# Performance work log

Measured on AMD Instinct MI355X. Metric: run time of the kernel, lower is better.

Reference implementation:

```python
import jax, jax.numpy as jnp
import numpy as np

N_SPEC = 256
M_IN = 16384
K_OUT = 4096


def _get_edges(wl):
    # bin edges at midpoints, extrapolated half a bin at each end
    mid = (wl[1:] + wl[:-1]) / 2
    first = wl[0] - (wl[1] - wl[0]) / 2
    last = wl[-1] + (wl[-1] - wl[-2]) / 2
    return jnp.concatenate([first[None], mid, last[None]])


def setup_inputs() -> dict:
    key = jax.random.key(0)
    k1, = jax.random.split(key, 1)
    # strictly increasing wavelength grids (nm); output grid coarser and inside input range
    wl_in = jnp.linspace(400.0, 900.0, M_IN, dtype=jnp.float32)
    wl_out = jnp.linspace(405.0, 895.0, K_OUT, dtype=jnp.float32)
    flux_in = jax.random.uniform(k1, (N_SPEC, M_IN), dtype=jnp.float32, minval=0.1, maxval=1.0)
    return {"wl_in": wl_in, "flux_in": flux_in, "wl_out": wl_out}


def reference(wl_in, flux_in, wl_out):
    # Flux-conserving rebinning (Spectrum.resample with method='conserve').
    edges_in = _get_edges(wl_in)    # (M+1,)
    edges_out = _get_edges(wl_out)  # (K+1,)
    delta_in = edges_in[1:] - edges_in[:-1]    # (M,)
    delta_out = edges_out[1:] - edges_out[:-1]  # (K,)
    # overlap length between each output bin k and input bin m -> (K, M)
    overlap_lo = jnp.maximum(edges_out[:-1, None], edges_in[None, :-1])
    overlap_hi = jnp.minimum(edges_out[1:, None], edges_in[None, 1:])
    overlap = jnp.clip(overlap_hi - overlap_lo, 0, None)
    frac = overlap / delta_in[None, :]  # fraction of input bin m landing in output bin k
    # sum_m flux[n,m] * frac[k,m] * delta_in[m]  (contraction instead of the (N,K,M) broadcast)
    w = frac * delta_in[None, :]  # (K, M)
    flux_out = jnp.einsum('nm,km->nk', flux_in, w) / delta_out[None, :]
    return flux_out
```

## Files before the change

kernel.cpp:

```cpp
#include <hip/hip_runtime.h>


#define MAXW 6
#define NPB  8

__device__ __forceinline__ float edge_at(const float* __restrict__ wl, int n, int m) {
    if (m <= 0) return wl[0] - 0.5f * (wl[1] - wl[0]);
    if (m >= n) return wl[n - 1] + 0.5f * (wl[n - 1] - wl[n - 2]);
    return 0.5f * (wl[m - 1] + wl[m]);
}

__global__ __launch_bounds__(256) void rebin_kernel(
    const float* __restrict__ wl_in, const float* __restrict__ flux_in,
    const float* __restrict__ wl_out, float* __restrict__ out,
    int M, int K, int N)
{
    int k = blockIdx.x * blockDim.x + threadIdx.x;
    if (k >= K) return;

    float eo_lo = edge_at(wl_out, K, k);
    float eo_hi = edge_at(wl_out, K, k + 1);
    float inv_d = 1.0f / (eo_hi - eo_lo);

    int lo = 0, hi = M;
    while (lo < hi) {
        int mid = (lo + hi) >> 1;
        if (edge_at(wl_in, M, mid + 1) <= eo_lo) lo = mid + 1; else hi = mid;
    }
    int m0 = lo;

    float w[MAXW];
    int   mi[MAXW];
    #pragma unroll
    for (int j = 0; j < MAXW; ++j) {
        int m = m0 + j;
        float ww = 0.0f;
        if (m < M) {
            float a = edge_at(wl_in, M, m);
            float b = edge_at(wl_in, M, m + 1);
            ww = fmaxf(fminf(eo_hi, b) - fmaxf(eo_lo, a), 0.0f) * inv_d;
        }
        w[j]  = ww;
        mi[j] = (m < M) ? m : (M - 1);
    }

    int n0   = blockIdx.y * NPB;
    int nend = min(n0 + NPB, N);
    for (int n = n0; n < nend; ++n) {
        const float* fr = flux_in + (size_t)n * M;
        float acc = 0.0f;
        #pragma unroll
        for (int j = 0; j < MAXW; ++j) acc = fmaf(fr[mi[j]], w[j], acc);
        out[(size_t)n * K + k] = acc;
    }
}

extern "C" void kernel_launch(void* const* d_in, const int* in_sizes, int n_in,
                              void* d_out, int out_size, void* d_ws, size_t ws_size,
                              hipStream_t stream) {
    const float* wl_in   = (const float*)d_in[0];
    const float* flux_in = (const float*)d_in[1];
    const float* wl_out  = (const float*)d_in[2];
    float* out = (float*)d_out;

    int M = in_sizes[0];
    int K = in_sizes[2];
    int N = in_sizes[1] / M;

    dim3 block(256);
    dim3 grid((K + 255) / 256, (N + NPB - 1) / NPB);
    rebin_kernel<<<grid, block, 0, stream>>>(wl_in, flux_in, wl_out, out, M, K, N);
}
```

Measured before the change: 77.02 us.

## Replace binary search with arithmetic bin estimate and vectorized aligned loads

Computes the starting input bin from an assumed uniform spacing, then corrects it with short linear walks instead of a dependent-load binary search. Weights are built over an 8-wide window aligned to 4 so flux can be read with two float4 loads. Rows per block drop from 8 to 2 to raise parallelism, at the cost of repeating per-thread setup more often. The walks stay correct for non-uniform grids but could get long there.

Measured after the change: 73.34 us. -4.8%, faster.

```diff
diff --git a/kernel.cpp b/kernel.cpp
--- a/kernel.cpp
+++ b/kernel.cpp
@@ -1,8 +1,7 @@
 #include <hip/hip_runtime.h>
 
 
-#define MAXW 6
-#define NPB  8
+#define NPB 2
 
 __device__ __forceinline__ float edge_at(const float* __restrict__ wl, int n, int m) {
     if (m <= 0) return wl[0] - 0.5f * (wl[1] - wl[0]);
@@ -10,7 +9,7 @@
     return 0.5f * (wl[m - 1] + wl[m]);
 }
 
-__global__ __launch_bounds__(256) void rebin_kernel(
+__global__ __launch_bounds__(256) void rebin_v2_kernel(
     const float* __restrict__ wl_in, const float* __restrict__ flux_in,
     const float* __restrict__ wl_out, float* __restrict__ out,
     int M, int K, int N)
@@ -22,35 +21,51 @@
     float eo_hi = edge_at(wl_out, K, k + 1);
     float inv_d = 1.0f / (eo_hi - eo_lo);
 
-    int lo = 0, hi = M;
-    while (lo < hi) {
-        int mid = (lo + hi) >> 1;
-        if (edge_at(wl_in, M, mid + 1) <= eo_lo) lo = mid + 1; else hi = mid;
-    }
-    int m0 = lo;
+    float w0 = wl_in[0];
+    float e0 = w0 - 0.5f * (wl_in[1] - w0);
+    float spacing = (wl_in[M - 1] - w0) / (float)(M - 1);
+    int m0 = (int)floorf((eo_lo - e0) / spacing);
+    m0 = max(0, min(M - 1, m0));
+    while (m0 > 0 && edge_at(wl_in, M, m0) > eo_lo) --m0;
+    while (m0 < M - 1 && edge_at(wl_in, M, m0 + 1) <= eo_lo) ++m0;
 
-    float w[MAXW];
-    int   mi[MAXW];
+    int abase = m0 & ~3;
+
+    float wa[8];
+    float e_prev = edge_at(wl_in, M, abase);
     #pragma unroll
-    for (int j = 0; j < MAXW; ++j) {
-        int m = m0 + j;
-        float ww = 0.0f;
-        if (m < M) {
-            float a = edge_at(wl_in, M, m);
-            float b = edge_at(wl_in, M, m + 1);
-            ww = fmaxf(fminf(eo_hi, b) - fmaxf(eo_lo, a), 0.0f) * inv_d;
-        }
-        w[j]  = ww;
-        mi[j] = (m < M) ? m : (M - 1);
+    for (int t = 0; t < 8; ++t) {
+        float e_next = edge_at(wl_in, M, abase + t + 1);
+        float ov = fminf(eo_hi, e_next) - fmaxf(eo_lo, e_prev);
+        wa[t] = fmaxf(ov, 0.0f) * inv_d;
+        e_prev = e_next;
     }
 
     int n0   = blockIdx.y * NPB;
     int nend = min(n0 + NPB, N);
+    bool fast = (abase + 8 <= M);
     for (int n = n0; n < nend; ++n) {
         const float* fr = flux_in + (size_t)n * M;
-        float acc = 0.0f;
-        #pragma unroll
-        for (int j = 0; j < MAXW; ++j) acc = fmaf(fr[mi[j]], w[j], acc);
+        float acc;
+        if (fast) {
+            float4 f0 = *reinterpret_cast<const float4*>(fr + abase);
+            float4 f1 = *reinterpret_cast<const float4*>(fr + abase + 4);
+            acc = f0.x * wa[0];
+            acc = fmaf(f0.y, wa[1], acc);
+            acc = fmaf(f0.z, wa[2], acc);
+            acc = fmaf(f0.w, wa[3], acc);
+            acc = fmaf(f1.x, wa[4], acc);
+            acc = fmaf(f1.y, wa[5], acc);
+            acc = fmaf(f1.z, wa[6], acc);
+            acc = fmaf(f1.w, wa[7], acc);
+        } else {
+            acc = 0.0f;
+            #pragma unroll
+            for (int t = 0; t < 8; ++t) {
+                int idx = min(abase + t, M - 1);
+                acc = fmaf(fr[idx], wa[t], acc);
+            }
+        }
         out[(size_t)n * K + k] = acc;
     }
 }
@@ -69,5 +84,5 @@
 
     dim3 block(256);
     dim3 grid((K + 255) / 256, (N + NPB - 1) / NPB);
-    rebin_kernel<<<grid, block, 0, stream>>>(wl_in, flux_in, wl_out, out, M, K, N);
+    rebin_v2_kernel<<<grid, block, 0, stream>>>(wl_in, flux_in, wl_out, out, M, K, N);
 }
```
